# Optimization experiments

Hardware: AMD Instinct MI355X
Metric: run time of the kernel (lower is better)

Reference implementation:

```python
import jax, jax.numpy as jnp
import numpy as np


def _chamfer(pred, tgt):
    # pred: [B,N,3], tgt: [B,M,3]
    # Euclidean pairwise distances (same math as torch.cdist, p=2)
    p2 = jnp.sum(pred * pred, axis=-1)              # [B,N]
    t2 = jnp.sum(tgt * tgt, axis=-1)                # [B,M]
    cross = jnp.einsum('bnd,bmd->bnm', pred, tgt)   # [B,N,M]
    sq = p2[:, :, None] + t2[:, None, :] - 2.0 * cross
    dist = jnp.sqrt(jnp.maximum(sq, 0.0))           # [B,N,M]
    min_p2t = jnp.min(dist, axis=2)                 # [B,N]
    min_t2p = jnp.min(dist, axis=1)                 # [B,M]
    return jnp.mean(min_p2t) + jnp.mean(min_t2p)


def setup_inputs() -> dict:
    key = jax.random.key(0)
    k1, k2 = jax.random.split(key)
    B, N, M, D = 8, 4096, 4096, 3
    predicted_points = jax.random.normal(k1, (B, N, D), dtype=jnp.float32)
    target_points = jax.random.normal(k2, (B, M, D), dtype=jnp.float32)
    return {"predicted_points": predicted_points, "target_points": target_points}


def reference(predicted_points, target_points):
    return _chamfer(predicted_points, target_points)
```

## Files before the change

kernel.cpp:

```cpp
#include <hip/hip_runtime.h>
#include <math.h>

#define B_SZ 8
#define N_SZ 4096
#define M_SZ 4096
#define NQ (B_SZ * N_SZ)
#define TOT (2 * NQ)

#define THREADS 256
#define QPT 8
#define QPB (THREADS * QPT)
#define ITILES (N_SZ / QPB)
#define JTILE 256
#define NJT (M_SZ / JTILE)
#define JPAIRS (JTILE / 2)

#define NBLK2 (TOT / 256)

__global__ __launch_bounds__(THREADS)
void chamfer_partial_kernel(const float* __restrict__ pred,
                            const float* __restrict__ tgt,
                            float* __restrict__ part)
{
    const int b   = blockIdx.y;
    const int dir = blockIdx.z;

    const float* Q;
    const float* Db;
    int qoff;
    if (dir == 0) { Q = pred + (size_t)b * N_SZ * 3; Db = tgt  + (size_t)b * M_SZ * 3; qoff = b * N_SZ; }
    else          { Q = tgt  + (size_t)b * M_SZ * 3; Db = pred + (size_t)b * N_SZ * 3; qoff = NQ + b * M_SZ; }

    const int itile = blockIdx.x >> 4;
    const int g     = blockIdx.x & (NJT - 1);

    __shared__ float4 sp[JTILE];
    {
        const float* s = Db + (size_t)(g * JTILE + threadIdx.x) * 3;
        float x = s[0], y = s[1], z = s[2];
        sp[threadIdx.x] = make_float4(x, y, z, 0.5f * (x * x + y * y + z * z));
    }
    __syncthreads();

    float qxn[QPT], qyn[QPT], qzn[QPT], q2h[QPT], mn[QPT];
    const int qbase = itile * QPB + threadIdx.x;
#pragma unroll
    for (int i = 0; i < QPT; ++i) {
        const int qi = qbase + i * THREADS;
        float x = Q[qi * 3 + 0], y = Q[qi * 3 + 1], z = Q[qi * 3 + 2];
        qxn[i] = -x;
        qyn[i] = -y;
        qzn[i] = -z;
        q2h[i] = 0.5f * (x * x + y * y + z * z);
        mn[i]  = 3.0e38f;
    }

#pragma unroll 4
    for (int jp = 0; jp < JPAIRS; ++jp) {
        float4 t0 = sp[2 * jp];
        float4 t1 = sp[2 * jp + 1];
#pragma unroll
        for (int i = 0; i < QPT; ++i) {
            float s0 = fmaf(qxn[i], t0.x, t0.w);
            s0 = fmaf(qyn[i], t0.y, s0);
            s0 = fmaf(qzn[i], t0.z, s0);
            float s1 = fmaf(qxn[i], t1.x, t1.w);
            s1 = fmaf(qyn[i], t1.y, s1);
            s1 = fmaf(qzn[i], t1.z, s1);
            asm("v_min3_f32 %0, %1, %2, %3"
                : "=v"(mn[i]) : "v"(mn[i]), "v"(s0), "v"(s1));
        }
    }

    float* pg = part + (size_t)g * TOT + qoff;
#pragma unroll
    for (int i = 0; i < QPT; ++i)
        pg[qbase + i * THREADS] = mn[i] + q2h[i];
}

__global__ __launch_bounds__(256)
void chamfer_combine_kernel(const float* __restrict__ part,
                            float* __restrict__ bsum)
{
    const int q = blockIdx.x * 256 + threadIdx.x;
    float m = 3.0e38f;
#pragma unroll
    for (int g = 0; g < NJT; ++g) m = fminf(m, part[(size_t)g * TOT + q]);
    float d = sqrtf(2.0f * fmaxf(m, 0.0f));
#pragma unroll
    for (int off = 32; off > 0; off >>= 1) d += __shfl_down(d, off);
    __shared__ float r[4];
    if ((threadIdx.x & 63) == 0) r[threadIdx.x >> 6] = d;
    __syncthreads();
    if (threadIdx.x == 0) bsum[blockIdx.x] = r[0] + r[1] + r[2] + r[3];
}

__global__ __launch_bounds__(64)
void chamfer_final_kernel(const float* __restrict__ bsum,
                          float* __restrict__ out)
{
    float s = 0.0f;
#pragma unroll
    for (int i = 0; i < NBLK2 / 64; ++i) s += bsum[threadIdx.x + i * 64];
#pragma unroll
    for (int off = 32; off > 0; off >>= 1) s += __shfl_down(s, off);
    if (threadIdx.x == 0) out[0] = s * (1.0f / (float)NQ);
}

extern "C" void kernel_launch(void* const* d_in, const int* in_sizes, int n_in,
                              void* d_out, int out_size, void* d_ws, size_t ws_size,
                              hipStream_t stream) {
    const float* pred = (const float*)d_in[0];
    const float* tgt  = (const float*)d_in[1];
    float* out = (float*)d_out;

    float* part = (float*)d_ws;
    float* bsum = part + (size_t)NJT * TOT;

    dim3 grid1(ITILES * NJT, B_SZ, 2);
    chamfer_partial_kernel<<<grid1, THREADS, 0, stream>>>(pred, tgt, part);
    chamfer_combine_kernel<<<NBLK2, 256, 0, stream>>>(part, bsum);
    chamfer_final_kernel<<<1, 64, 0, stream>>>(bsum, out);
}
```

Measured before the change: 81.77 us.

## Compute both chamfer directions from one shared distance tile per block

Each distance value is now computed once and used for both the row-min and the column-min, where before it was computed separately for each direction. Each block takes a 128x128 query/target tile and uses an 8x8 register micro-tile per thread. Shared-memory reductions then produce partial minima for both directions. This roughly halves the FMA work but adds an extra add per pair for column mins, shared-memory reduction traffic, and a larger partial buffer (32 slices instead of 16) for the combine kernel to read.

```diff
diff --git a/kernel.cpp b/kernel.cpp
--- a/kernel.cpp
+++ b/kernel.cpp
@@ -7,75 +7,116 @@
 #define NQ (B_SZ * N_SZ)
 #define TOT (2 * NQ)
 
-#define THREADS 256
-#define QPT 8
-#define QPB (THREADS * QPT)
-#define ITILES (N_SZ / QPB)
-#define JTILE 256
-#define NJT (M_SZ / JTILE)
-#define JPAIRS (JTILE / 2)
+#define BQ 128
+#define BT 128
+#define NIG (N_SZ / BQ)
+#define NJG (M_SZ / BT)
+#define NG  32
 
 #define NBLK2 (TOT / 256)
 
-__global__ __launch_bounds__(THREADS)
-void chamfer_partial_kernel(const float* __restrict__ pred,
-                            const float* __restrict__ tgt,
-                            float* __restrict__ part)
+
+__device__ __forceinline__ float min3f(float a, float b, float c) {
+    float d;
+    asm("v_min3_f32 %0, %1, %2, %3" : "=v"(d) : "v"(a), "v"(b), "v"(c));
+    return d;
+}
+
+__global__ __launch_bounds__(256)
+void chamfer_cross_kernel(const float* __restrict__ pred,
+                          const float* __restrict__ tgt,
+                          float* __restrict__ part)
 {
-    const int b   = blockIdx.y;
-    const int dir = blockIdx.z;
+    const int b  = blockIdx.z;
+    const int ig = blockIdx.y;
+    const int jg = blockIdx.x;
 
-    const float* Q;
-    const float* Db;
-    int qoff;
-    if (dir == 0) { Q = pred + (size_t)b * N_SZ * 3; Db = tgt  + (size_t)b * M_SZ * 3; qoff = b * N_SZ; }
-    else          { Q = tgt  + (size_t)b * M_SZ * 3; Db = pred + (size_t)b * N_SZ * 3; qoff = NQ + b * M_SZ; }
+    __shared__ float4 sq[BQ];
+    __shared__ float4 st[BT];
+    __shared__ float  redR[BQ][17];
+    __shared__ float  redC[BT][17];
 
-    const int itile = blockIdx.x >> 4;
-    const int g     = blockIdx.x & (NJT - 1);
-
-    __shared__ float4 sp[JTILE];
     {
-        const float* s = Db + (size_t)(g * JTILE + threadIdx.x) * 3;
-        float x = s[0], y = s[1], z = s[2];
-        sp[threadIdx.x] = make_float4(x, y, z, 0.5f * (x * x + y * y + z * z));
+        const int k = threadIdx.x;
+        if (k < BQ) {
+            const float* s = pred + ((size_t)b * N_SZ + ig * BQ + k) * 3;
+            float x = s[0], y = s[1], z = s[2];
+            sq[k] = make_float4(x, y, z, 0.5f * (x * x + y * y + z * z));
+        } else {
+            const int k2 = k - BQ;
+            const float* s = tgt + ((size_t)b * M_SZ + jg * BT + k2) * 3;
+            float x = s[0], y = s[1], z = s[2];
+            st[k2] = make_float4(x, y, z, 0.5f * (x * x + y * y + z * z));
+        }
     }
     __syncthreads();
 
-    float qxn[QPT], qyn[QPT], qzn[QPT], q2h[QPT], mn[QPT];
-    const int qbase = itile * QPB + threadIdx.x;
+    const int r = threadIdx.x >> 4;
+    const int c = threadIdx.x & 15;
+
+    float qxn[8], qyn[8], qzn[8], hq[8];
+    float tx[8], ty[8], tz[8], ht[8];
 #pragma unroll
-    for (int i = 0; i < QPT; ++i) {
-        const int qi = qbase + i * THREADS;
-        float x = Q[qi * 3 + 0], y = Q[qi * 3 + 1], z = Q[qi * 3 + 2];
-        qxn[i] = -x;
-        qyn[i] = -y;
-        qzn[i] = -z;
-        q2h[i] = 0.5f * (x * x + y * y + z * z);
-        mn[i]  = 3.0e38f;
+    for (int i = 0; i < 8; ++i) {
+        float4 v = sq[r * 8 + i];
+        qxn[i] = -v.x; qyn[i] = -v.y; qzn[i] = -v.z; hq[i] = v.w;
+    }
+#pragma unroll
+    for (int j = 0; j < 8; ++j) {
+        float4 v = st[c * 8 + j];
+        tx[j] = v.x; ty[j] = v.y; tz[j] = v.z; ht[j] = v.w;
     }
 
-#pragma unroll 4
-    for (int jp = 0; jp < JPAIRS; ++jp) {
-        float4 t0 = sp[2 * jp];
-        float4 t1 = sp[2 * jp + 1];
+    float mr[8], mc[8];
 #pragma unroll
-        for (int i = 0; i < QPT; ++i) {
-            float s0 = fmaf(qxn[i], t0.x, t0.w);
-            s0 = fmaf(qyn[i], t0.y, s0);
-            s0 = fmaf(qzn[i], t0.z, s0);
-            float s1 = fmaf(qxn[i], t1.x, t1.w);
-            s1 = fmaf(qyn[i], t1.y, s1);
-            s1 = fmaf(qzn[i], t1.z, s1);
-            asm("v_min3_f32 %0, %1, %2, %3"
-                : "=v"(mn[i]) : "v"(mn[i]), "v"(s0), "v"(s1));
+    for (int i = 0; i < 8; ++i) { mr[i] = 3.0e38f; mc[i] = 3.0e38f; }
+
+#pragma unroll
+    for (int j = 0; j < 8; j += 2) {
+#pragma unroll
+        for (int i = 0; i < 8; i += 2) {
+            float r00 = fmaf(qxn[i],     tx[j],     ht[j]);
+            r00 = fmaf(qyn[i],     ty[j],     r00);
+            r00 = fmaf(qzn[i],     tz[j],     r00);
+            float r01 = fmaf(qxn[i],     tx[j + 1], ht[j + 1]);
+            r01 = fmaf(qyn[i],     ty[j + 1], r01);
+            r01 = fmaf(qzn[i],     tz[j + 1], r01);
+            float r10 = fmaf(qxn[i + 1], tx[j],     ht[j]);
+            r10 = fmaf(qyn[i + 1], ty[j],     r10);
+            r10 = fmaf(qzn[i + 1], tz[j],     r10);
+            float r11 = fmaf(qxn[i + 1], tx[j + 1], ht[j + 1]);
+            r11 = fmaf(qyn[i + 1], ty[j + 1], r11);
+            r11 = fmaf(qzn[i + 1], tz[j + 1], r11);
+            mr[i]     = min3f(mr[i],     r00, r01);
+            mr[i + 1] = min3f(mr[i + 1], r10, r11);
+            float c00 = r00 + hq[i];
+            float c10 = r10 + hq[i + 1];
+            mc[j]     = min3f(mc[j],     c00, c10);
+            float c01 = r01 + hq[i];
+            float c11 = r11 + hq[i + 1];
+            mc[j + 1] = min3f(mc[j + 1], c01, c11);
         }
     }
 
-    float* pg = part + (size_t)g * TOT + qoff;
 #pragma unroll
-    for (int i = 0; i < QPT; ++i)
-        pg[qbase + i * THREADS] = mn[i] + q2h[i];
+    for (int i = 0; i < 8; ++i) redR[r * 8 + i][c] = mr[i] + hq[i];
+#pragma unroll
+    for (int j = 0; j < 8; ++j) redC[c * 8 + j][r] = mc[j];
+    __syncthreads();
+
+    const int tid = threadIdx.x;
+    if (tid < BQ) {
+        float m = 3.0e38f;
+#pragma unroll
+        for (int k = 0; k < 16; ++k) m = fminf(m, redR[tid][k]);
+        part[(size_t)jg * TOT + (size_t)b * N_SZ + ig * BQ + tid] = m;
+    } else {
+        const int t = tid - BQ;
+        float m = 3.0e38f;
+#pragma unroll
+        for (int k = 0; k < 16; ++k) m = fminf(m, redC[t][k]);
+        part[(size_t)ig * TOT + NQ + (size_t)b * M_SZ + jg * BT + t] = m;
+    }
 }
 
 __global__ __launch_bounds__(256)
@@ -85,14 +126,14 @@
     const int q = blockIdx.x * 256 + threadIdx.x;
     float m = 3.0e38f;
 #pragma unroll
-    for (int g = 0; g < NJT; ++g) m = fminf(m, part[(size_t)g * TOT + q]);
+    for (int g = 0; g < NG; ++g) m = fminf(m, part[(size_t)g * TOT + q]);
     float d = sqrtf(2.0f * fmaxf(m, 0.0f));
 #pragma unroll
     for (int off = 32; off > 0; off >>= 1) d += __shfl_down(d, off);
-    __shared__ float r[4];
-    if ((threadIdx.x & 63) == 0) r[threadIdx.x >> 6] = d;
+    __shared__ float rs[4];
+    if ((threadIdx.x & 63) == 0) rs[threadIdx.x >> 6] = d;
     __syncthreads();
-    if (threadIdx.x == 0) bsum[blockIdx.x] = r[0] + r[1] + r[2] + r[3];
+    if (threadIdx.x == 0) bsum[blockIdx.x] = rs[0] + rs[1] + rs[2] + rs[3];
 }
 
 __global__ __launch_bounds__(64)
@@ -115,10 +156,10 @@
     float* out = (float*)d_out;
 
     float* part = (float*)d_ws;
-    float* bsum = part + (size_t)NJT * TOT;
+    float* bsum = part + (size_t)NG * TOT;
 
-    dim3 grid1(ITILES * NJT, B_SZ, 2);
-    chamfer_partial_kernel<<<grid1, THREADS, 0, stream>>>(pred, tgt, part);
+    dim3 grid1(NJG, NIG, B_SZ);
+    chamfer_cross_kernel<<<grid1, 256, 0, stream>>>(pred, tgt, part);
     chamfer_combine_kernel<<<NBLK2, 256, 0, stream>>>(part, bsum);
     chamfer_final_kernel<<<1, 64, 0, stream>>>(bsum, out);
 }
```

Result: slower. 86.81 us (+6.2%).

## Fuse partial, combine and final kernels into one cooperative launch with grid syncs

Applied to the files above, without the earlier changes.

Merges the three-kernel pipeline (partial min, per-query combine, final sum) into a single cooperative kernel that uses grid-wide syncs between stages. The aim is to remove two kernel launch gaps and their inter-kernel drain and fill. The cost is two grid barriers over 512 blocks, and the cooperative launch needs every block to be resident at once, which can fail or limit occupancy.

```diff
diff --git a/kernel.cpp b/kernel.cpp
--- a/kernel.cpp
+++ b/kernel.cpp
@@ -1,5 +1,8 @@
 #include <hip/hip_runtime.h>
+#include <hip/hip_cooperative_groups.h>
 #include <math.h>
+
+namespace cg = cooperative_groups;
 
 #define B_SZ 8
 #define N_SZ 4096
@@ -15,15 +18,27 @@
 #define NJT (M_SZ / JTILE)
 #define JPAIRS (JTILE / 2)
 
+#define NBLK1 (ITILES * NJT * B_SZ * 2)
 #define NBLK2 (TOT / 256)
 
+
+__device__ __forceinline__ float min3f(float a, float b, float c) {
+    float d;
+    asm("v_min3_f32 %0, %1, %2, %3" : "=v"(d) : "v"(a), "v"(b), "v"(c));
+    return d;
+}
+
 __global__ __launch_bounds__(THREADS)
-void chamfer_partial_kernel(const float* __restrict__ pred,
-                            const float* __restrict__ tgt,
-                            float* __restrict__ part)
+void chamfer_fused_kernel(const float* __restrict__ pred,
+                          const float* __restrict__ tgt,
+                          float* __restrict__ part,
+                          float* __restrict__ bsum,
+                          float* __restrict__ out)
 {
     const int b   = blockIdx.y;
     const int dir = blockIdx.z;
+    const int tid = threadIdx.x;
+    const int fb  = blockIdx.x + (ITILES * NJT) * (b + B_SZ * dir);
 
     const float* Q;
     const float* Db;
@@ -36,14 +51,14 @@
 
     __shared__ float4 sp[JTILE];
     {
-        const float* s = Db + (size_t)(g * JTILE + threadIdx.x) * 3;
+        const float* s = Db + (size_t)(g * JTILE + tid) * 3;
         float x = s[0], y = s[1], z = s[2];
-        sp[threadIdx.x] = make_float4(x, y, z, 0.5f * (x * x + y * y + z * z));
+        sp[tid] = make_float4(x, y, z, 0.5f * (x * x + y * y + z * z));
     }
     __syncthreads();
 
     float qxn[QPT], qyn[QPT], qzn[QPT], q2h[QPT], mn[QPT];
-    const int qbase = itile * QPB + threadIdx.x;
+    const int qbase = itile * QPB + tid;
 #pragma unroll
     for (int i = 0; i < QPT; ++i) {
         const int qi = qbase + i * THREADS;
@@ -67,44 +82,43 @@
             float s1 = fmaf(qxn[i], t1.x, t1.w);
             s1 = fmaf(qyn[i], t1.y, s1);
             s1 = fmaf(qzn[i], t1.z, s1);
-            asm("v_min3_f32 %0, %1, %2, %3"
-                : "=v"(mn[i]) : "v"(mn[i]), "v"(s0), "v"(s1));
+            mn[i] = min3f(mn[i], s0, s1);
         }
     }
 
-    float* pg = part + (size_t)g * TOT + qoff;
+    {
+        float* pg = part + (size_t)g * TOT + qoff;
 #pragma unroll
-    for (int i = 0; i < QPT; ++i)
-        pg[qbase + i * THREADS] = mn[i] + q2h[i];
-}
+        for (int i = 0; i < QPT; ++i)
+            pg[qbase + i * THREADS] = mn[i] + q2h[i];
+    }
 
-__global__ __launch_bounds__(256)
-void chamfer_combine_kernel(const float* __restrict__ part,
-                            float* __restrict__ bsum)
-{
-    const int q = blockIdx.x * 256 + threadIdx.x;
-    float m = 3.0e38f;
+    __threadfence();
+    cg::this_grid().sync();
+
+    __shared__ float rs[4];
+    if (fb < NBLK2) {
+        const int q = fb * 256 + tid;
+        float m = 3.0e38f;
 #pragma unroll
-    for (int g = 0; g < NJT; ++g) m = fminf(m, part[(size_t)g * TOT + q]);
-    float d = sqrtf(2.0f * fmaxf(m, 0.0f));
+        for (int gg = 0; gg < NJT; ++gg) m = fminf(m, part[(size_t)gg * TOT + q]);
+        float d = sqrtf(2.0f * fmaxf(m, 0.0f));
 #pragma unroll
-    for (int off = 32; off > 0; off >>= 1) d += __shfl_down(d, off);
-    __shared__ float r[4];
-    if ((threadIdx.x & 63) == 0) r[threadIdx.x >> 6] = d;
-    __syncthreads();
-    if (threadIdx.x == 0) bsum[blockIdx.x] = r[0] + r[1] + r[2] + r[3];
-}
+        for (int off = 32; off > 0; off >>= 1) d += __shfl_down(d, off);
+        if ((tid & 63) == 0) rs[tid >> 6] = d;
+        __syncthreads();
+        if (tid == 0) bsum[fb] = rs[0] + rs[1] + rs[2] + rs[3];
+    }
 
-__global__ __launch_bounds__(64)
-void chamfer_final_kernel(const float* __restrict__ bsum,
-                          float* __restrict__ out)
-{
-    float s = 0.0f;
+    __threadfence();
+    cg::this_grid().sync();
+
+    if (fb == 0 && tid < 64) {
+        float s = bsum[tid] + bsum[tid + 64] + bsum[tid + 128] + bsum[tid + 192];
 #pragma unroll
-    for (int i = 0; i < NBLK2 / 64; ++i) s += bsum[threadIdx.x + i * 64];
-#pragma unroll
-    for (int off = 32; off > 0; off >>= 1) s += __shfl_down(s, off);
-    if (threadIdx.x == 0) out[0] = s * (1.0f / (float)NQ);
+        for (int off = 32; off > 0; off >>= 1) s += __shfl_down(s, off);
+        if (tid == 0) out[0] = s * (1.0f / (float)NQ);
+    }
 }
 
 extern "C" void kernel_launch(void* const* d_in, const int* in_sizes, int n_in,
@@ -118,7 +132,9 @@
     float* bsum = part + (size_t)NJT * TOT;
 
     dim3 grid1(ITILES * NJT, B_SZ, 2);
-    chamfer_partial_kernel<<<grid1, THREADS, 0, stream>>>(pred, tgt, part);
-    chamfer_combine_kernel<<<NBLK2, 256, 0, stream>>>(part, bsum);
-    chamfer_final_kernel<<<1, 64, 0, stream>>>(bsum, out);
+    dim3 blk(THREADS, 1, 1);
+    void* args[] = { (void*)&pred, (void*)&tgt, (void*)&part,
+                     (void*)&bsum, (void*)&out };
+    hipLaunchCooperativeKernel((const void*)chamfer_fused_kernel,
+                               grid1, blk, args, 0, stream);
 }
```

Measured after the change: 248.1 us. 3.03x slower.
